# Optimization experiments

Hardware: AMD Instinct MI355X
Metric: run time of the kernel (lower is better)

The kernel has to match this reference:

```python
import jax, jax.numpy as jnp
import numpy as np


def _make_dplr_hippo(N):
    # Standard HiPPO-LegS -> NPLR -> DPLR construction (Annotated S4).
    p = np.sqrt(1.0 + 2.0 * np.arange(N))
    A = p[:, None] * p[None, :]
    A = np.tril(A) - np.diag(np.arange(N))
    A = -A
    P = np.sqrt(np.arange(N) + 0.5)
    B = np.sqrt(2.0 * np.arange(N) + 1.0)
    # Normal part S = A + P P^T is skew-symmetric + const*I
    S = A + P[:, None] * P[None, :]
    Lambda_real = np.mean(np.diagonal(S)) * np.ones(N)  # = -0.5
    Lambda_imag, V = np.linalg.eigh(S * -1j)            # S*-1j is Hermitian
    Lambda = Lambda_real + 1j * Lambda_imag
    Pc = V.conj().T @ P
    Bc = V.conj().T @ B
    return Lambda, Pc, Bc


N_STATE = 64
SEQ_LEN = 16384
BATCH = 1024


def setup_inputs() -> dict:
    key = jax.random.key(0)
    kx, kcr, kci = jax.random.split(key, 3)
    Lambda, P, B = _make_dplr_hippo(N_STATE)
    scale = 0.5 ** 0.5
    return {
        "x": jax.random.normal(kx, (BATCH, SEQ_LEN), dtype=jnp.float32),
        "Lambda_real": jnp.asarray(Lambda.real, dtype=jnp.float32),
        "Lambda_imag": jnp.asarray(Lambda.imag, dtype=jnp.float32),
        "P_real": jnp.asarray(P.real, dtype=jnp.float32),
        "P_imag": jnp.asarray(P.imag, dtype=jnp.float32),
        "B_real": jnp.asarray(B.real, dtype=jnp.float32),
        "B_imag": jnp.asarray(B.imag, dtype=jnp.float32),
        "C_real": jax.random.normal(kcr, (N_STATE,), dtype=jnp.float32) * scale,
        "C_imag": jax.random.normal(kci, (N_STATE,), dtype=jnp.float32) * scale,
        "step_size": jnp.asarray(0.01, dtype=jnp.float32),
    }


def _s4_fourier_kernel(Lambda, P, Q, B, C, step, L):
    # Evaluate the DPLR SSM generating function at the L roots of unity
    # via 4 Cauchy dot products (the classic S4 bottleneck).
    k = jnp.arange(L, dtype=jnp.float32)
    Omega = jnp.exp(-2j * jnp.pi * k / L)                 # [L] complex64
    g = (2.0 / step) * (1.0 - Omega) / (1.0 + Omega)      # [L]
    c = 2.0 / (1.0 + Omega)                               # [L]
    inv = 1.0 / (g[:, None] - Lambda[None, :])            # [L, N] Cauchy denominators
    a0 = jnp.conj(C)
    a1 = jnp.conj(Q)
    k00 = inv @ (a0 * B)   # [L]
    k01 = inv @ (a0 * P)
    k10 = inv @ (a1 * B)
    k11 = inv @ (a1 * P)
    return c * (k00 - k01 * (1.0 / (1.0 + k11)) * k10)    # [L]


def reference(x, Lambda_real, Lambda_imag, P_real, P_imag, B_real, B_imag,
              C_real, C_imag, step_size):
    L = x.shape[-1]
    Lambda = Lambda_real + 1j * Lambda_imag
    P = P_real + 1j * P_imag
    B = B_real + 1j * B_imag
    C_tilde = C_real + 1j * C_imag
    # Original computes the kernel under torch.no_grad().
    kernel = _s4_fourier_kernel(Lambda, P, P, B, C_tilde, step_size, L)  # [L]
    fft_u = jnp.fft.fft(x, n=L)              # [batch, L] complex64
    y = jnp.fft.ifft(kernel * fft_u, n=L)    # circular conv in freq domain
    return y.real
```

## Files before the change

kernel.cpp:

```cpp
#include <hip/hip_runtime.h>
#include <math.h>

#define LFFT 16384
#define MFFT 8192
#define NT   512
#define PITCH 17

#define LDS_FENCE() asm volatile("s_waitcnt lgkmcnt(0)" ::: "memory")

__device__ __forceinline__ float2 cadd(float2 a, float2 b){ return make_float2(a.x+b.x, a.y+b.y); }
__device__ __forceinline__ float2 csub(float2 a, float2 b){ return make_float2(a.x-b.x, a.y-b.y); }
__device__ __forceinline__ float2 cmul(float2 a, float2 b){ return make_float2(a.x*b.x - a.y*b.y, a.x*b.y + a.y*b.x); }
__device__ __forceinline__ float2 cmulc(float2 a, float2 b){ return make_float2(a.x*b.x + a.y*b.y, a.y*b.x - a.x*b.y); }

template<int S> __device__ __forceinline__ float2 mul_is(float2 a) {
    return make_float2(-(float)S * a.y, (float)S * a.x);
}

template<int S> __device__ __forceinline__ void dft4_t(float2& a0, float2& a1, float2& a2, float2& a3) {
    float2 t0 = cadd(a0, a2);
    float2 t1 = csub(a0, a2);
    float2 t2 = cadd(a1, a3);
    float2 t3 = csub(a1, a3);
    a0 = cadd(t0, t2);
    a2 = csub(t0, t2);
    const float s = (float)S;
    a1 = make_float2(t1.x - s * t3.y, t1.y + s * t3.x);
    a3 = make_float2(t1.x + s * t3.y, t1.y - s * t3.x);
}

#define C16A 0.92387953251128675613f
#define C16B 0.70710678118654752440f
#define C16C 0.38268343236508977173f

template<int S> __device__ __forceinline__ void dft16_t(float2 r[16]) {
    const float s = (float)S;
    const float2 w1 = make_float2( C16A, s * C16C);
    const float2 w2 = make_float2( C16B, s * C16B);
    const float2 w3 = make_float2( C16C, s * C16A);
    const float2 w6 = make_float2(-C16B, s * C16B);
    const float2 w9 = make_float2(-C16A, -s * C16C);
    float2 g[4][4];
    #pragma unroll
    for (int b = 0; b < 4; ++b) {
        float2 a0 = r[b], a1 = r[b+4], a2 = r[b+8], a3 = r[b+12];
        dft4_t<S>(a0, a1, a2, a3);
        g[b][0] = a0; g[b][1] = a1; g[b][2] = a2; g[b][3] = a3;
    }
    g[1][1] = cmul(g[1][1], w1);  g[1][2] = cmul(g[1][2], w2);  g[1][3] = cmul(g[1][3], w3);
    g[2][1] = cmul(g[2][1], w2);  g[2][2] = mul_is<S>(g[2][2]); g[2][3] = cmul(g[2][3], w6);
    g[3][1] = cmul(g[3][1], w3);  g[3][2] = cmul(g[3][2], w6);  g[3][3] = cmul(g[3][3], w9);
    #pragma unroll
    for (int ka = 0; ka < 4; ++ka) {
        float2 a0 = g[0][ka], a1 = g[1][ka], a2 = g[2][ka], a3 = g[3][ka];
        dft4_t<S>(a0, a1, a2, a3);
        r[ka] = a0; r[ka+4] = a1; r[ka+8] = a2; r[ka+12] = a3;
    }
}

__device__ __forceinline__ void twiddle15(float2 r[16], float2 w) {
    float2 w2 = cmul(w, w);
    float2 we = w2;
    float2 wo = cmul(w, w2);
    r[1] = cmul(r[1], w);
    r[2] = cmul(r[2], we);
    r[3] = cmul(r[3], wo);
    #pragma unroll
    for (int j = 2; j <= 7; ++j) {
        we = cmul(we, w2);  r[2*j]   = cmul(r[2*j],   we);
        wo = cmul(wo, w2);  r[2*j+1] = cmul(r[2*j+1], wo);
    }
}

__global__ void s4_eval(const float* __restrict__ Lr, const float* __restrict__ Li,
                        const float* __restrict__ Pr, const float* __restrict__ Pi,
                        const float* __restrict__ Br, const float* __restrict__ Bi,
                        const float* __restrict__ Cr, const float* __restrict__ Ci,
                        const float* __restrict__ step_ptr,
                        float2* __restrict__ Kraw, float2* __restrict__ twidM)
{
    int m = blockIdx.x * blockDim.x + threadIdx.x;
    if (m >= LFFT) return;
    if (m < MFFT) {
        double th2 = (-2.0 * M_PI / (double)MFFT) * (double)m;
        double s2, c2;
        sincos(th2, &s2, &c2);
        twidM[m] = make_float2((float)c2, (float)s2);
    }
    double theta = (-2.0 * M_PI / (double)LFFT) * (double)m;
    double si, co;
    sincos(theta, &si, &co);

    double step = (double)step_ptr[0];
    double opr = 1.0 + co, opi = si;
    double omr = 1.0 - co, omi = -si;
    double iden = 1.0 / (opr*opr + opi*opi);
    double gs = 2.0 / step;
    double gr = gs * (omr*opr + omi*opi) * iden;
    double gi = gs * (omi*opr - omr*opi) * iden;
    double cr = 2.0 * opr * iden;
    double ci = -2.0 * opi * iden;

    double k00r=0,k00i=0,k01r=0,k01i=0,k10r=0,k10i=0,k11r=0,k11i=0;
    for (int n = 0; n < 64; ++n) {
        double dr = gr - (double)Lr[n];
        double di = gi - (double)Li[n];
        double id2 = 1.0 / (dr*dr + di*di);
        double vr =  dr * id2;
        double vi = -di * id2;
        double a0r = (double)Cr[n], a0i = -(double)Ci[n];
        double a1r = (double)Pr[n], a1i = -(double)Pi[n];
        double br  = (double)Br[n], bi  = (double)Bi[n];
        double pr  = (double)Pr[n], pi  = (double)Pi[n];
        double e00r = a0r*br - a0i*bi, e00i = a0r*bi + a0i*br;
        double e01r = a0r*pr - a0i*pi, e01i = a0r*pi + a0i*pr;
        double e10r = a1r*br - a1i*bi, e10i = a1r*bi + a1i*br;
        double e11r = a1r*pr - a1i*pi, e11i = a1r*pi + a1i*pr;
        k00r += vr*e00r - vi*e00i;  k00i += vr*e00i + vi*e00r;
        k01r += vr*e01r - vi*e01i;  k01i += vr*e01i + vi*e01r;
        k10r += vr*e10r - vi*e10i;  k10i += vr*e10i + vi*e10r;
        k11r += vr*e11r - vi*e11i;  k11i += vr*e11i + vi*e11r;
    }
    double rr = 1.0 + k11r, ri = k11i;
    double ir2 = 1.0 / (rr*rr + ri*ri);
    double qr0 = k01r*k10r - k01i*k10i;
    double qi0 = k01r*k10i + k01i*k10r;
    double qr = (qr0*rr + qi0*ri) * ir2;
    double qi = (qi0*rr - qr0*ri) * ir2;
    double sr = k00r - qr, sim = k00i - qi;
    Kraw[m] = make_float2((float)(cr*sr - ci*sim), (float)(cr*sim + ci*sr));
}

__global__ void s4_uv(const float2* __restrict__ Kraw, float4* __restrict__ UV)
{
    int p = blockIdx.x * blockDim.x + threadIdx.x;
    if (p >= MFFT) return;
    int t = p >> 4, j = p & 15;
    int k = (t >> 5) | (((t >> 1) & 15) << 4) | (j << 8) | ((t & 1) << 12);

    float2 Ka = Kraw[k];
    float2 Kb = Kraw[(LFFT - k) & (LFFT - 1)];
    float2 Kc = Kraw[k + MFFT];
    float2 Kd = Kraw[MFFT - k];
    double ar = 0.5 * ((double)Ka.x + (double)Kb.x);
    double ai = 0.5 * ((double)Ka.y - (double)Kb.y);
    double br = 0.5 * ((double)Kc.x + (double)Kd.x);
    double bi = 0.5 * ((double)Kc.y - (double)Kd.y);
    double Pr = 0.5 * (ar + br), Pi = 0.5 * (ai + bi);
    double Qr = 0.5 * (ar - br), Qi = 0.5 * (ai - bi);
    double th = (2.0 * M_PI / (double)LFFT) * (double)k;
    double sn, cs;
    sincos(th, &sn, &cs);
    double inv = 1.0 / (double)MFFT;
    double Ur = (Pr - sn * Qr) * inv, Ui = (Pi - sn * Qi) * inv;
    double Vr = (-cs * Qi) * inv,     Vi = ( cs * Qr) * inv;
    UV[p] = make_float4((float)Ur, (float)Ui, (float)Vr, (float)Vi);
}

__global__ __launch_bounds__(NT, 4) void fft_conv(
    const float* __restrict__ x, float* __restrict__ y,
    const float2* __restrict__ twidM, const float4* __restrict__ UV)
{
    __shared__ float2 lds[NT * PITCH];
    const int t = threadIdx.x;
    const int u = t & 31;
    const int g = t >> 5;
    const size_t base = (size_t)blockIdx.x * LFFT;
    const float2* xz = (const float2*)(x + base);

    float2 r[16];
    #pragma unroll
    for (int a = 0; a < 16; ++a) r[a] = xz[t + NT*a];

    dft16_t<-1>(r);
    twiddle15(r, twidM[t]);

    #pragma unroll
    for (int k = 0; k < 16; ++k)
        lds[(32*k + u) * PITCH + g] = r[k];
    __syncthreads();
    #pragma unroll
    for (int b = 0; b < 16; ++b) r[b] = lds[t * PITCH + b];
    LDS_FENCE();

    dft16_t<-1>(r);
    twiddle15(r, twidM[16 * u]);

    #pragma unroll
    for (int k = 0; k < 16; ++k)
        lds[((t & ~31) + 2*k + (t & 1)) * PITCH + (u >> 1)] = r[k];
    LDS_FENCE();
    #pragma unroll
    for (int m = 0; m < 16; ++m) r[m] = lds[t * PITCH + m];
    LDS_FENCE();

    dft16_t<-1>(r);
    twiddle15(r, twidM[256 * (t & 1)]);

    #pragma unroll
    for (int j = 0; j < 16; ++j) {
        float2 o;
        o.x = __shfl_xor(r[j].x, 1);
        o.y = __shfl_xor(r[j].y, 1);
        r[j] = (t & 1) ? csub(o, r[j]) : cadd(r[j], o);
    }

    #pragma unroll
    for (int j = 0; j < 16; ++j) lds[t * PITCH + j] = r[j];
    __syncthreads();
    {
        const float4* uv = UV + t * 16;
        const int kb = g | (((t >> 1) & 15) << 4) | ((t & 1) << 12);
        #pragma unroll
        for (int j = 0; j < 16; ++j) {
            int k  = kb + (j << 8);
            int kp = (MFFT - k) & (MFFT - 1);
            int tp = ((kp & 15) << 5) | (((kp >> 4) & 15) << 1) | (kp >> 12);
            int cp = (kp >> 8) & 15;
            float2 zp = lds[tp * PITCH + cp];
            float4 c  = uv[j];
            r[j] = cadd(cmul(make_float2(c.x, c.y), r[j]),
                        cmulc(make_float2(c.z, c.w), zp));
        }
    }
    __syncthreads();

    #pragma unroll
    for (int j = 0; j < 16; ++j) {
        float2 o;
        o.x = __shfl_xor(r[j].x, 1);
        o.y = __shfl_xor(r[j].y, 1);
        r[j] = (t & 1) ? csub(o, r[j]) : cadd(r[j], o);
    }
    { float2 w0 = twidM[256 * (t & 1)]; twiddle15(r, make_float2(w0.x, -w0.y)); }
    dft16_t<1>(r);

    #pragma unroll
    for (int m = 0; m < 16; ++m)
        lds[((t & ~31) + (t & 1) + 2*m) * PITCH + (u >> 1)] = r[m];
    LDS_FENCE();
    #pragma unroll
    for (int k = 0; k < 16; ++k) r[k] = lds[t * PITCH + k];

    { float2 w0 = twidM[16 * u]; twiddle15(r, make_float2(w0.x, -w0.y)); }
    dft16_t<1>(r);

    __syncthreads();
    #pragma unroll
    for (int b = 0; b < 16; ++b)
        lds[(u + 32*b) * PITCH + g] = r[b];
    __syncthreads();
    #pragma unroll
    for (int k = 0; k < 16; ++k) r[k] = lds[t * PITCH + k];

    { float2 w0 = twidM[t]; twiddle15(r, make_float2(w0.x, -w0.y)); }
    dft16_t<1>(r);

    float2* yz = (float2*)(y + base);
    #pragma unroll
    for (int a = 0; a < 16; ++a) yz[t + NT*a] = r[a];
}

extern "C" void kernel_launch(void* const* d_in, const int* in_sizes, int n_in,
                              void* d_out, int out_size, void* d_ws, size_t ws_size,
                              hipStream_t stream)
{
    const float* x  = (const float*)d_in[0];
    const float* Lr = (const float*)d_in[1];
    const float* Li = (const float*)d_in[2];
    const float* Pr = (const float*)d_in[3];
    const float* Pi = (const float*)d_in[4];
    const float* Br = (const float*)d_in[5];
    const float* Bi = (const float*)d_in[6];
    const float* Cr = (const float*)d_in[7];
    const float* Ci = (const float*)d_in[8];
    const float* st = (const float*)d_in[9];

    const int rows = in_sizes[0] / LFFT;

    float2* Kraw  = (float2*)d_ws;
    float2* twidM = Kraw + LFFT;
    float4* UV    = (float4*)(twidM + MFFT);

    s4_eval<<<LFFT / 64, 64, 0, stream>>>(Lr, Li, Pr, Pi, Br, Bi, Cr, Ci, st,
                                          Kraw, twidM);
    s4_uv<<<MFFT / 64, 64, 0, stream>>>(Kraw, UV);
    fft_conv<<<rows, NT, 0, stream>>>(x, (float*)d_out, twidM, UV);
}
```

Baseline: 77.09 us.

## Prefetch next row via async global_load_lds and fuse kernel-table setup

Each block of the FFT convolution kernel now handles four rows. While the current row is being transformed, the next row is streamed directly into an LDS staging buffer with global_load_lds, so global loads overlap with compute. The LDS pitch changes to 18 so transpose reads can use float4 loads, and the two setup kernels are merged into one that builds the Cauchy kernel values and the UV table through shared memory. The costs are lower occupancy (launch bounds drop to 2 and LDS use grows), only 256 blocks for 1024 rows, and hand-written vmcnt waits that must match the number of outstanding loads exactly.

```diff
diff --git a/kernel.cpp b/kernel.cpp
--- a/kernel.cpp
+++ b/kernel.cpp
@@ -4,9 +4,13 @@
 #define LFFT 16384
 #define MFFT 8192
 #define NT   512
-#define PITCH 17
+#define PITCH 18
+#define NROWS_PER_BLK 4
 
 #define LDS_FENCE() asm volatile("s_waitcnt lgkmcnt(0)" ::: "memory")
+
+typedef const __attribute__((address_space(1))) unsigned int glob_u32;
+typedef __attribute__((address_space(3))) unsigned int lds_u32;
 
 __device__ __forceinline__ float2 cadd(float2 a, float2 b){ return make_float2(a.x+b.x, a.y+b.y); }
 __device__ __forceinline__ float2 csub(float2 a, float2 b){ return make_float2(a.x-b.x, a.y-b.y); }
@@ -72,26 +76,15 @@
     }
 }
 
-__global__ void s4_eval(const float* __restrict__ Lr, const float* __restrict__ Li,
+__device__ float2 evalK(int m, double step,
+                        const float* __restrict__ Lr, const float* __restrict__ Li,
                         const float* __restrict__ Pr, const float* __restrict__ Pi,
                         const float* __restrict__ Br, const float* __restrict__ Bi,
-                        const float* __restrict__ Cr, const float* __restrict__ Ci,
-                        const float* __restrict__ step_ptr,
-                        float2* __restrict__ Kraw, float2* __restrict__ twidM)
-{
-    int m = blockIdx.x * blockDim.x + threadIdx.x;
-    if (m >= LFFT) return;
-    if (m < MFFT) {
-        double th2 = (-2.0 * M_PI / (double)MFFT) * (double)m;
-        double s2, c2;
-        sincos(th2, &s2, &c2);
-        twidM[m] = make_float2((float)c2, (float)s2);
-    }
+                        const float* __restrict__ Cr, const float* __restrict__ Ci)
+{
     double theta = (-2.0 * M_PI / (double)LFFT) * (double)m;
     double si, co;
     sincos(theta, &si, &co);
-
-    double step = (double)step_ptr[0];
     double opr = 1.0 + co, opi = si;
     double omr = 1.0 - co, omi = -si;
     double iden = 1.0 / (opr*opr + opi*opi);
@@ -128,137 +121,220 @@
     double qr = (qr0*rr + qi0*ri) * ir2;
     double qi = (qi0*rr - qr0*ri) * ir2;
     double sr = k00r - qr, sim = k00i - qi;
-    Kraw[m] = make_float2((float)(cr*sr - ci*sim), (float)(cr*sim + ci*sr));
-}
-
-__global__ void s4_uv(const float2* __restrict__ Kraw, float4* __restrict__ UV)
-{
-    int p = blockIdx.x * blockDim.x + threadIdx.x;
-    if (p >= MFFT) return;
+    return make_float2((float)(cr*sr - ci*sim), (float)(cr*sim + ci*sr));
+}
+
+__global__ void s4_tables(const float* __restrict__ Lr, const float* __restrict__ Li,
+                          const float* __restrict__ Pr, const float* __restrict__ Pi,
+                          const float* __restrict__ Br, const float* __restrict__ Bi,
+                          const float* __restrict__ Cr, const float* __restrict__ Ci,
+                          const float* __restrict__ step_ptr,
+                          float4* __restrict__ UV, float2* __restrict__ twidM)
+{
+    __shared__ float2 vals[256];
+    const int tid = threadIdx.x;
+    const int T = blockIdx.x * 256 + tid;
+    const int p = T >> 2, c = T & 3;
+
+    if (T < MFFT) {
+        double th2 = (-2.0 * M_PI / (double)MFFT) * (double)T;
+        double s2, c2;
+        sincos(th2, &s2, &c2);
+        twidM[T] = make_float2((float)c2, (float)s2);
+    }
+
     int t = p >> 4, j = p & 15;
     int k = (t >> 5) | (((t >> 1) & 15) << 4) | (j << 8) | ((t & 1) << 12);
-
-    float2 Ka = Kraw[k];
-    float2 Kb = Kraw[(LFFT - k) & (LFFT - 1)];
-    float2 Kc = Kraw[k + MFFT];
-    float2 Kd = Kraw[MFFT - k];
-    double ar = 0.5 * ((double)Ka.x + (double)Kb.x);
-    double ai = 0.5 * ((double)Ka.y - (double)Kb.y);
-    double br = 0.5 * ((double)Kc.x + (double)Kd.x);
-    double bi = 0.5 * ((double)Kc.y - (double)Kd.y);
-    double Pr = 0.5 * (ar + br), Pi = 0.5 * (ai + bi);
-    double Qr = 0.5 * (ar - br), Qi = 0.5 * (ai - bi);
-    double th = (2.0 * M_PI / (double)LFFT) * (double)k;
-    double sn, cs;
-    sincos(th, &sn, &cs);
-    double inv = 1.0 / (double)MFFT;
-    double Ur = (Pr - sn * Qr) * inv, Ui = (Pi - sn * Qi) * inv;
-    double Vr = (-cs * Qi) * inv,     Vi = ( cs * Qr) * inv;
-    UV[p] = make_float4((float)Ur, (float)Ui, (float)Vr, (float)Vi);
-}
-
-__global__ __launch_bounds__(NT, 4) void fft_conv(
+    int idx;
+    if      (c == 0) idx = k;
+    else if (c == 1) idx = (LFFT - k) & (LFFT - 1);
+    else if (c == 2) idx = k + MFFT;
+    else             idx = MFFT - k;
+
+    double step = (double)step_ptr[0];
+    vals[tid] = evalK(idx, step, Lr, Li, Pr, Pi, Br, Bi, Cr, Ci);
+    __syncthreads();
+    if (c == 0) {
+        float2 Ka = vals[tid], Kb = vals[tid+1], Kc = vals[tid+2], Kd = vals[tid+3];
+        double ar = 0.5 * ((double)Ka.x + (double)Kb.x);
+        double ai = 0.5 * ((double)Ka.y - (double)Kb.y);
+        double br = 0.5 * ((double)Kc.x + (double)Kd.x);
+        double bi = 0.5 * ((double)Kc.y - (double)Kd.y);
+        double Pr2 = 0.5 * (ar + br), Pi2 = 0.5 * (ai + bi);
+        double Qr  = 0.5 * (ar - br), Qi  = 0.5 * (ai - bi);
+        double th = (2.0 * M_PI / (double)LFFT) * (double)k;
+        double sn, cs;
+        sincos(th, &sn, &cs);
+        double inv = 1.0 / (double)MFFT;
+        UV[p] = make_float4((float)((Pr2 - sn * Qr) * inv),
+                            (float)((Pi2 - sn * Qi) * inv),
+                            (float)((-cs * Qi) * inv),
+                            (float)(( cs * Qr) * inv));
+    }
+}
+
+__device__ __forceinline__ void stage_row(const float* __restrict__ xrow,
+                                          float2* stage, int wave, int lane)
+{
+    #pragma unroll
+    for (int c = 0; c < 8; ++c) {
+        const int chunk = wave * 8 + c;
+        const float* src = xrow + chunk * 256 + lane * 4;
+        float2* dst = stage + chunk * 128;
+        __builtin_amdgcn_global_load_lds((glob_u32*)src, (lds_u32*)dst, 16, 0, 0);
+    }
+}
+
+__global__ __launch_bounds__(NT, 2) void fft_conv(
     const float* __restrict__ x, float* __restrict__ y,
     const float2* __restrict__ twidM, const float4* __restrict__ UV)
 {
-    __shared__ float2 lds[NT * PITCH];
+    __shared__ float2 smem[MFFT + NT * PITCH];
+    float2* stage = smem;
+    float2* tbuf  = smem + MFFT;
     const int t = threadIdx.x;
     const int u = t & 31;
     const int g = t >> 5;
-    const size_t base = (size_t)blockIdx.x * LFFT;
-    const float2* xz = (const float2*)(x + base);
-
-    float2 r[16];
-    #pragma unroll
-    for (int a = 0; a < 16; ++a) r[a] = xz[t + NT*a];
-
-    dft16_t<-1>(r);
-    twiddle15(r, twidM[t]);
-
-    #pragma unroll
-    for (int k = 0; k < 16; ++k)
-        lds[(32*k + u) * PITCH + g] = r[k];
-    __syncthreads();
-    #pragma unroll
-    for (int b = 0; b < 16; ++b) r[b] = lds[t * PITCH + b];
-    LDS_FENCE();
-
-    dft16_t<-1>(r);
-    twiddle15(r, twidM[16 * u]);
-
-    #pragma unroll
-    for (int k = 0; k < 16; ++k)
-        lds[((t & ~31) + 2*k + (t & 1)) * PITCH + (u >> 1)] = r[k];
-    LDS_FENCE();
-    #pragma unroll
-    for (int m = 0; m < 16; ++m) r[m] = lds[t * PITCH + m];
-    LDS_FENCE();
-
-    dft16_t<-1>(r);
-    twiddle15(r, twidM[256 * (t & 1)]);
-
-    #pragma unroll
-    for (int j = 0; j < 16; ++j) {
-        float2 o;
-        o.x = __shfl_xor(r[j].x, 1);
-        o.y = __shfl_xor(r[j].y, 1);
-        r[j] = (t & 1) ? csub(o, r[j]) : cadd(r[j], o);
-    }
-
-    #pragma unroll
-    for (int j = 0; j < 16; ++j) lds[t * PITCH + j] = r[j];
-    __syncthreads();
-    {
-        const float4* uv = UV + t * 16;
-        const int kb = g | (((t >> 1) & 15) << 4) | ((t & 1) << 12);
+    const int wave = t >> 6, lane = t & 63;
+    const size_t blkbase = (size_t)blockIdx.x * NROWS_PER_BLK * LFFT;
+
+    stage_row(x + blkbase, stage, wave, lane);
+
+    for (int i = 0; i < NROWS_PER_BLK; ++i) {
+        const size_t base = blkbase + (size_t)i * LFFT;
+
+        if (i == 0) asm volatile("s_waitcnt vmcnt(0)" ::: "memory");
+        else        asm volatile("s_waitcnt vmcnt(16)" ::: "memory");
+        __syncthreads();
+
+        float2 r[16];
+        #pragma unroll
+        for (int a = 0; a < 16; ++a) r[a] = stage[t + NT*a];
+        LDS_FENCE();
+        __syncthreads();
+        if (i + 1 < NROWS_PER_BLK)
+            stage_row(x + base + LFFT, stage, wave, lane);
+
+        dft16_t<-1>(r);
+        twiddle15(r, twidM[t]);
+
+        #pragma unroll
+        for (int k = 0; k < 16; ++k)
+            tbuf[(32*k + u) * PITCH + g] = r[k];
+        __syncthreads();
+        {
+            const float4* row4 = (const float4*)(tbuf + t * PITCH);
+            #pragma unroll
+            for (int q = 0; q < 8; ++q) {
+                float4 v = row4[q];
+                r[2*q]   = make_float2(v.x, v.y);
+                r[2*q+1] = make_float2(v.z, v.w);
+            }
+        }
+        LDS_FENCE();
+
+        dft16_t<-1>(r);
+        twiddle15(r, twidM[16 * u]);
+
+        #pragma unroll
+        for (int k = 0; k < 16; ++k)
+            tbuf[((t & ~31) + 2*k + (t & 1)) * PITCH + (u >> 1)] = r[k];
+        LDS_FENCE();
+        {
+            const float4* row4 = (const float4*)(tbuf + t * PITCH);
+            #pragma unroll
+            for (int q = 0; q < 8; ++q) {
+                float4 v = row4[q];
+                r[2*q]   = make_float2(v.x, v.y);
+                r[2*q+1] = make_float2(v.z, v.w);
+            }
+        }
+        LDS_FENCE();
+
+        dft16_t<-1>(r);
+        twiddle15(r, twidM[256 * (t & 1)]);
+
         #pragma unroll
         for (int j = 0; j < 16; ++j) {
-            int k  = kb + (j << 8);
-            int kp = (MFFT - k) & (MFFT - 1);
-            int tp = ((kp & 15) << 5) | (((kp >> 4) & 15) << 1) | (kp >> 12);
-            int cp = (kp >> 8) & 15;
-            float2 zp = lds[tp * PITCH + cp];
-            float4 c  = uv[j];
-            r[j] = cadd(cmul(make_float2(c.x, c.y), r[j]),
-                        cmulc(make_float2(c.z, c.w), zp));
-        }
-    }
-    __syncthreads();
-
-    #pragma unroll
-    for (int j = 0; j < 16; ++j) {
-        float2 o;
-        o.x = __shfl_xor(r[j].x, 1);
-        o.y = __shfl_xor(r[j].y, 1);
-        r[j] = (t & 1) ? csub(o, r[j]) : cadd(r[j], o);
-    }
-    { float2 w0 = twidM[256 * (t & 1)]; twiddle15(r, make_float2(w0.x, -w0.y)); }
-    dft16_t<1>(r);
-
-    #pragma unroll
-    for (int m = 0; m < 16; ++m)
-        lds[((t & ~31) + (t & 1) + 2*m) * PITCH + (u >> 1)] = r[m];
-    LDS_FENCE();
-    #pragma unroll
-    for (int k = 0; k < 16; ++k) r[k] = lds[t * PITCH + k];
-
-    { float2 w0 = twidM[16 * u]; twiddle15(r, make_float2(w0.x, -w0.y)); }
-    dft16_t<1>(r);
-
-    __syncthreads();
-    #pragma unroll
-    for (int b = 0; b < 16; ++b)
-        lds[(u + 32*b) * PITCH + g] = r[b];
-    __syncthreads();
-    #pragma unroll
-    for (int k = 0; k < 16; ++k) r[k] = lds[t * PITCH + k];
-
-    { float2 w0 = twidM[t]; twiddle15(r, make_float2(w0.x, -w0.y)); }
-    dft16_t<1>(r);
-
-    float2* yz = (float2*)(y + base);
-    #pragma unroll
-    for (int a = 0; a < 16; ++a) yz[t + NT*a] = r[a];
+            float2 o;
+            o.x = __shfl_xor(r[j].x, 1);
+            o.y = __shfl_xor(r[j].y, 1);
+            r[j] = (t & 1) ? csub(o, r[j]) : cadd(r[j], o);
+        }
+
+        {
+            float4* row4w = (float4*)(tbuf + t * PITCH);
+            #pragma unroll
+            for (int q = 0; q < 8; ++q)
+                row4w[q] = make_float4(r[2*q].x, r[2*q].y, r[2*q+1].x, r[2*q+1].y);
+        }
+        __syncthreads();
+        {
+            const float4* uv = UV + t * 16;
+            const int kb = g | (((t >> 1) & 15) << 4) | ((t & 1) << 12);
+            #pragma unroll
+            for (int j = 0; j < 16; ++j) {
+                int k  = kb + (j << 8);
+                int kp = (MFFT - k) & (MFFT - 1);
+                int tp = ((kp & 15) << 5) | (((kp >> 4) & 15) << 1) | (kp >> 12);
+                int cp = (kp >> 8) & 15;
+                float2 zp = tbuf[tp * PITCH + cp];
+                float4 cc = uv[j];
+                r[j] = cadd(cmul(make_float2(cc.x, cc.y), r[j]),
+                            cmulc(make_float2(cc.z, cc.w), zp));
+            }
+        }
+        __syncthreads();
+
+        #pragma unroll
+        for (int j = 0; j < 16; ++j) {
+            float2 o;
+            o.x = __shfl_xor(r[j].x, 1);
+            o.y = __shfl_xor(r[j].y, 1);
+            r[j] = (t & 1) ? csub(o, r[j]) : cadd(r[j], o);
+        }
+        { float2 w0 = twidM[256 * (t & 1)]; twiddle15(r, make_float2(w0.x, -w0.y)); }
+        dft16_t<1>(r);
+
+        #pragma unroll
+        for (int m = 0; m < 16; ++m)
+            tbuf[((t & ~31) + (t & 1) + 2*m) * PITCH + (u >> 1)] = r[m];
+        LDS_FENCE();
+        {
+            const float4* row4 = (const float4*)(tbuf + t * PITCH);
+            #pragma unroll
+            for (int q = 0; q < 8; ++q) {
+                float4 v = row4[q];
+                r[2*q]   = make_float2(v.x, v.y);
+                r[2*q+1] = make_float2(v.z, v.w);
+            }
+        }
+
+        { float2 w0 = twidM[16 * u]; twiddle15(r, make_float2(w0.x, -w0.y)); }
+        dft16_t<1>(r);
+
+        __syncthreads();
+        #pragma unroll
+        for (int b = 0; b < 16; ++b)
+            tbuf[(u + 32*b) * PITCH + g] = r[b];
+        __syncthreads();
+        {
+            const float4* row4 = (const float4*)(tbuf + t * PITCH);
+            #pragma unroll
+            for (int q = 0; q < 8; ++q) {
+                float4 v = row4[q];
+                r[2*q]   = make_float2(v.x, v.y);
+                r[2*q+1] = make_float2(v.z, v.w);
+            }
+        }
+
+        { float2 w0 = twidM[t]; twiddle15(r, make_float2(w0.x, -w0.y)); }
+        dft16_t<1>(r);
+
+        float2* yz = (float2*)(y + base);
+        #pragma unroll
+        for (int a = 0; a < 16; ++a) yz[t + NT*a] = r[a];
+    }
 }
 
 extern "C" void kernel_launch(void* const* d_in, const int* in_sizes, int n_in,
@@ -278,12 +354,10 @@
 
     const int rows = in_sizes[0] / LFFT;
 
-    float2* Kraw  = (float2*)d_ws;
-    float2* twidM = Kraw + LFFT;
+    float2* twidM = (float2*)d_ws;
     float4* UV    = (float4*)(twidM + MFFT);
 
-    s4_eval<<<LFFT / 64, 64, 0, stream>>>(Lr, Li, Pr, Pi, Br, Bi, Cr, Ci, st,
-                                          Kraw, twidM);
-    s4_uv<<<MFFT / 64, 64, 0, stream>>>(Kraw, UV);
-    fft_conv<<<rows, NT, 0, stream>>>(x, (float*)d_out, twidM, UV);
-}
+    s4_tables<<<(4 * MFFT) / 256, 256, 0, stream>>>(Lr, Li, Pr, Pi, Br, Bi,
+                                                    Cr, Ci, st, UV, twidM);
+    fft_conv<<<rows / NROWS_PER_BLK, NT, 0, stream>>>(x, (float*)d_out, twidM, UV);
+}
```

After: 87.37 us. 13.3% more time.
